# Kernel optimization log

Measured on AMD Instinct MI355X. Metric: run time of the kernel, lower is better.

The kernel has to match this reference:

```python
import jax, jax.numpy as jnp
import numpy as np

HEADS = 16
DIM_HEAD = 64
MASK_VALUE = -(np.finfo(np.float32).max / 2)


def setup_inputs() -> dict:
    key = jax.random.key(0)
    k1, k2, k3 = jax.random.split(key, 3)
    B, N, D = 2, 2048, 1024
    inner = HEADS * DIM_HEAD
    x = jax.random.normal(k1, (B, N, D), dtype=jnp.float32)
    w_qkv = jax.random.normal(k2, (D, 3 * inner), dtype=jnp.float32) * (D ** -0.5)
    w_out = jax.random.normal(k3, (inner, D), dtype=jnp.float32) * (inner ** -0.5)
    b_out = jnp.zeros((D,), dtype=jnp.float32)
    return {"x": x, "w_qkv": w_qkv, "w_out": w_out, "b_out": b_out}


def reference(x, w_qkv, w_out, b_out):
    B, N, D = x.shape
    H, Dh = HEADS, DIM_HEAD
    qkv = x @ w_qkv                                   # [B, N, 3*H*Dh]
    q, k, v = jnp.split(qkv, 3, axis=-1)
    # [B, N, H*Dh] -> [B, H, N, Dh]
    split_heads = lambda t: t.reshape(B, N, H, Dh).transpose(0, 2, 1, 3)
    q, k, v = split_heads(q), split_heads(k), split_heads(v)
    scale = Dh ** -0.5
    sim = jnp.einsum('bhid,bhjd->bhij', q, k) * scale  # [B, H, N, N]
    # causal additive mask: MASK_VALUE above the diagonal
    causal = jnp.triu(jnp.ones((N, N), dtype=bool), k=1)
    mask = jnp.where(causal, jnp.float32(MASK_VALUE), 0.0)
    sim = sim + mask[None, None, :, :]
    attn = jax.nn.softmax(sim, axis=-1)
    out = jnp.einsum('bhij,bhjd->bhid', attn, v)       # [B, H, N, Dh]
    out = out.transpose(0, 2, 1, 3).reshape(B, N, H * Dh)
    return out @ w_out + b_out
```

## Files before the change

### kernel.cpp

```cpp
#include <hip/hip_runtime.h>
#include <hip/hip_bf16.h>

typedef __attribute__((ext_vector_type(4)))  float    f32x4;
typedef __attribute__((ext_vector_type(16))) float    f32x16;
typedef __attribute__((ext_vector_type(8)))  short    bf16x8;
typedef __attribute__((ext_vector_type(4)))  short    s16x4;
typedef __attribute__((ext_vector_type(4)))  unsigned u32x4;

#define B_    2
#define N_    2048
#define D_    1024
#define HEADS 16
#define DH    64
#define M_    4096
#define INNER 1024

static __device__ __forceinline__ short f2bf(float f) {
    __hip_bfloat16 h = __float2bfloat16(f);
    return __builtin_bit_cast(short, h);
}
static __device__ __forceinline__ float bf2f(short s) {
    unsigned u = ((unsigned)(unsigned short)s) << 16;
    return __builtin_bit_cast(float, u);
}
static __device__ __forceinline__ unsigned pack2(float lo, float hi) {
    return ((unsigned)(unsigned short)f2bf(lo)) |
           (((unsigned)(unsigned short)f2bf(hi)) << 16);
}
static __device__ __forceinline__ unsigned cvtpk(float lo, float hi) {
    unsigned r;
    asm("v_cvt_pk_bf16_f32 %0, %1, %2" : "=v"(r) : "v"(lo), "v"(hi));
    return r;
}
static __device__ __forceinline__ void plswap(unsigned& a, unsigned& b) {
    asm("v_permlane32_swap_b32 %0, %1" : "+v"(a), "+v"(b));
}
static __device__ __forceinline__ float fexp2(float x) {
    float r;
    asm("v_exp_f32 %0, %1" : "=v"(r) : "v"(x));
    return r;
}
static __device__ __forceinline__ float flog2(float x) {
    float r;
    asm("v_log_f32 %0, %1" : "=v"(r) : "v"(x));
    return r;
}
static __device__ __forceinline__ float vmax16(f32x16 v) {
    float a = fmaxf(fmaxf(v[0], v[1]), fmaxf(v[2], v[3]));
    float b = fmaxf(fmaxf(v[4], v[5]), fmaxf(v[6], v[7]));
    float c = fmaxf(fmaxf(v[8], v[9]), fmaxf(v[10], v[11]));
    float d = fmaxf(fmaxf(v[12], v[13]), fmaxf(v[14], v[15]));
    return fmaxf(fmaxf(a, b), fmaxf(c, d));
}
static __device__ __forceinline__ float vsum16(f32x16 v) {
    float a = (v[0] + v[1]) + (v[2] + v[3]);
    float b = (v[4] + v[5]) + (v[6] + v[7]);
    float c = (v[8] + v[9]) + (v[10] + v[11]);
    float d = (v[12] + v[13]) + (v[14] + v[15]);
    return (a + b) + (c + d);
}

static __device__ __forceinline__ void transpose_tile(const float* __restrict__ in,
                                                      short* __restrict__ out,
                                                      int R, int C, int bx32, int by32,
                                                      float* t ) {
    int tx = threadIdx.x & 31, ty = threadIdx.x >> 5;
    int bx = bx32 * 32, by = by32 * 32;
#pragma unroll
    for (int j = 0; j < 32; j += 8)
        t[(ty + j) * 33 + tx] = in[(long)(by + ty + j) * C + bx + tx];
    __syncthreads();
#pragma unroll
    for (int j = 0; j < 32; j += 8)
        out[(long)(bx + ty + j) * R + by + tx] = f2bf(t[tx * 33 + ty + j]);
}

__global__ void __launch_bounds__(256) prep_k(const float* __restrict__ x,
                                              short* __restrict__ xb,
                                              const float* __restrict__ w_qkv,
                                              short* __restrict__ wqkvT,
                                              const float* __restrict__ w_out,
                                              short* __restrict__ woutT) {
    __shared__ float t[32 * 33];
    int bid = blockIdx.x;
    if (bid < 4096) {
        int i = bid * 256 + threadIdx.x;
        f32x4 v = ((const f32x4*)x)[i];
        s16x4 o;
        o[0] = f2bf(v[0]); o[1] = f2bf(v[1]); o[2] = f2bf(v[2]); o[3] = f2bf(v[3]);
        ((s16x4*)xb)[i] = o;
    } else if (bid < 4096 + 3072) {
        int tt = bid - 4096;
        transpose_tile(w_qkv, wqkvT, 1024, 3072, tt % 96, tt / 96, t);
    } else {
        int tt = bid - 7168;
        transpose_tile(w_out, woutT, 1024, 1024, tt % 32, tt / 32, t);
    }
}

template <int ROWS>
static __device__ __forceinline__ void stage_swz(const short* __restrict__ src,
                                                 int ldElems, short* lds, int tid) {
    constexpr int CH = (ROWS * 128) / (256 * 16);
#pragma unroll
    for (int c = 0; c < CH; ++c) {
        int o   = (tid + c * 256) * 16;
        int row = o >> 7;
        int kb  = (o & 127) ^ ((row & 7) << 4);
        const char* g = (const char*)src + (long)row * ldElems * 2 + kb;
        __builtin_amdgcn_global_load_lds(
            (const __attribute__((address_space(1))) void*)g,
            (__attribute__((address_space(3))) void*)((char*)lds + o), 16, 0, 0);
    }
}
static __device__ __forceinline__ bf16x8 lds_frag(const short* lds, int row, int kbyte) {
    return *(const bf16x8*)((const char*)lds + (row << 7) + (kbyte ^ ((row & 7) << 4)));
}

__global__ void __launch_bounds__(256) gemm_k(const short* __restrict__ A,
                                              const short* __restrict__ Bt, int K,
                                              short* __restrict__ q_out,
                                              short* __restrict__ k_out,
                                              short* __restrict__ v_out) {
    __shared__ __align__(16) short As[128 * 64];
    __shared__ __align__(16) short Bs[128 * 64];
    int tid = threadIdx.x;
    int lane = tid & 63, w = tid >> 6, wr = w >> 1, wc = w & 1;
    int l15 = lane & 15, lg = lane >> 4;
    int nx = gridDim.x;
    int flat = blockIdx.y * nx + blockIdx.x;
    int total = nx * gridDim.y;
    int cpx = total >> 3;
    int swz = (flat & 7) * cpx + (flat >> 3);
    int row0 = (swz / nx) * 128, col0 = (swz % nx) * 128;

    f32x4 acc[4][4] = {};

    for (int k0 = 0; k0 < K; k0 += 64) {
        stage_swz<128>(A + (long)row0 * K + k0, K, As, tid);
        stage_swz<128>(Bt + (long)col0 * K + k0, K, Bs, tid);
        __syncthreads();
#pragma unroll
        for (int kb = 0; kb < 2; ++kb) {
            int kbyte = kb * 64 + (lg << 4);
            bf16x8 af[4], bfr[4];
#pragma unroll
            for (int mr = 0; mr < 4; ++mr)
                af[mr] = lds_frag(As, wr * 64 + mr * 16 + l15, kbyte);
#pragma unroll
            for (int nr = 0; nr < 4; ++nr)
                bfr[nr] = lds_frag(Bs, wc * 64 + nr * 16 + l15, kbyte);
#pragma unroll
            for (int mr = 0; mr < 4; ++mr)
#pragma unroll
                for (int nr = 0; nr < 4; ++nr)
                    acc[mr][nr] = __builtin_amdgcn_mfma_f32_16x16x32_bf16(
                        af[mr], bfr[nr], acc[mr][nr], 0, 0, 0);
        }
        __syncthreads();
    }

#pragma unroll
    for (int mr = 0; mr < 4; ++mr)
#pragma unroll
        for (int nr = 0; nr < 4; ++nr) {
            int gr0 = row0 + wr * 64 + mr * 16 + (lg << 2);
            int gc  = col0 + wc * 64 + nr * 16 + l15;
            int which = gc >> 10, rem = gc & 1023;
            int h = rem >> 6, d = rem & 63;
            int b = gr0 >> 11, nn0 = gr0 & 2047;
            long bh32 = (long)(b * HEADS + h) * 32;
            if (which == 2) {
                int t = nn0 >> 6, ks = (nn0 >> 4) & 3, hb = (nn0 >> 3) & 1;
                long off = (((bh32 + t) * 2 + (d >> 5)) * 4 + ks) * 512
                           + ((hb << 5) + (d & 31)) * 8 + (nn0 & 4);
                s16x4 pk;
#pragma unroll
                for (int reg = 0; reg < 4; ++reg) pk[reg] = f2bf(acc[mr][nr][reg]);
                *(s16x4*)(v_out + off) = pk;
            } else if (which == 1) {
                int dk = d >> 4, hb = (d >> 3) & 1, j = d & 7;
                int t = nn0 >> 6, ss = (nn0 >> 5) & 1;
                long fbase = ((bh32 + t) * 2 + ss) * 4 + dk;
#pragma unroll
                for (int reg = 0; reg < 4; ++reg) {
                    int l31k = (nn0 + reg) & 31;
                    k_out[fbase * 512 + ((hb << 5) + l31k) * 8 + j] =
                        f2bf(acc[mr][nr][reg]);
                }
            } else {
                float sc = 0.180336880f;
#pragma unroll
                for (int reg = 0; reg < 4; ++reg) {
                    int gr = gr0 + reg;
                    int bb = gr >> 11, nn = gr & 2047;
                    q_out[((long)(bb * HEADS + h) * N_ + nn) * DH + d] =
                        f2bf(acc[mr][nr][reg] * sc);
                }
            }
        }
}

__global__ void __launch_bounds__(256) gemm2_k(const short* __restrict__ A,
                                               const short* __restrict__ Bt,
                                               float* __restrict__ f_out,
                                               const float* __restrict__ bias) {
    __shared__ __align__(16) short As[128 * 64];
    __shared__ __align__(16) short Bs[64 * 64];
    int tid = threadIdx.x;
    int lane = tid & 63, w = tid >> 6, wr = w >> 1, wc = w & 1;
    int l15 = lane & 15, lg = lane >> 4;
    const int K = 1024;
    int flat = blockIdx.y * 16 + blockIdx.x;
    int swz = (flat & 7) * 64 + (flat >> 3);
    int row0 = (swz >> 4) * 128, col0 = (swz & 15) * 64;

    f32x4 acc[4][2] = {};

    for (int k0 = 0; k0 < K; k0 += 64) {
        stage_swz<128>(A + (long)row0 * K + k0, K, As, tid);
        stage_swz<64>(Bt + (long)col0 * K + k0, K, Bs, tid);
        __syncthreads();
#pragma unroll
        for (int kb = 0; kb < 2; ++kb) {
            int kbyte = kb * 64 + (lg << 4);
            bf16x8 af[4], bfr[2];
#pragma unroll
            for (int mr = 0; mr < 4; ++mr)
                af[mr] = lds_frag(As, wr * 64 + mr * 16 + l15, kbyte);
#pragma unroll
            for (int nc = 0; nc < 2; ++nc)
                bfr[nc] = lds_frag(Bs, wc * 32 + nc * 16 + l15, kbyte);
#pragma unroll
            for (int mr = 0; mr < 4; ++mr)
#pragma unroll
                for (int nc = 0; nc < 2; ++nc)
                    acc[mr][nc] = __builtin_amdgcn_mfma_f32_16x16x32_bf16(
                        af[mr], bfr[nc], acc[mr][nc], 0, 0, 0);
        }
        __syncthreads();
    }

#pragma unroll
    for (int mr = 0; mr < 4; ++mr)
#pragma unroll
        for (int nc = 0; nc < 2; ++nc) {
            int gc = col0 + wc * 32 + nc * 16 + l15;
            float bv = bias[gc];
#pragma unroll
            for (int reg = 0; reg < 4; ++reg) {
                int gr = row0 + wr * 64 + mr * 16 + (lg << 2) + reg;
                f_out[(long)gr * D_ + gc] = acc[mr][nc][reg] + bv;
            }
        }
}

__global__ void __launch_bounds__(256, 3) attn_k(const short* __restrict__ Qb,
                                                 const short* __restrict__ Kf,
                                                 const short* __restrict__ Vf,
                                                 short* __restrict__ O0,
                                                 short* __restrict__ O1,
                                                 float* __restrict__ lse) {
    __shared__ __align__(16) short Ep[4][2048];
    int tid = threadIdx.x, lane = tid & 63, w = tid >> 6;
    int l31 = lane & 31, hbit = lane >> 5;
    int bid = blockIdx.x;
    int k8 = bid >> 3;
    int bh = (bid & 7) + ((k8 >> 5) << 3);
    int rest = k8 & 31;
    int q4 = rest >> 3, p = rest & 7;
    int x = (q4 < 2) ? (15 - p) : p;
    int seg = q4 & 1;
    int t0 = seg ? (x + 1) : 0;
    int t1 = seg ? (2 * x + 2) : (x + 1);

    const short* Qh = Qb + (long)bh * N_ * DH;
    const short* Kh = Kf + (long)bh * 32 * 4096;
    const short* Vh = Vf + (long)bh * 32 * 4096;
    int lofs = lane * 8;

    int q0 = x * 128 + w * 32;
    int qg = q0 + l31;
    int t1w = min(t1, ((q0 + 31) >> 6) + 1);

    bf16x8 qf[4];
#pragma unroll
    for (int kf = 0; kf < 4; ++kf)
        qf[kf] = *(const bf16x8*)(Qh + (long)qg * DH + kf * 16 + hbit * 8);

    f32x16 o[2] = {};
    float m = -1e30f, l = 0.f;

    for (int t = t0; t < t1w; ++t) {
        const short* kb = Kh + (long)t * 4096;
        const short* vb = Vh + (long)t * 4096;
        int khb = t * 64;

        bf16x8 kfr[2][4];
#pragma unroll
        for (int ss = 0; ss < 2; ++ss)
#pragma unroll
            for (int dk = 0; dk < 4; ++dk)
                kfr[ss][dk] = *(const bf16x8*)(kb + (ss * 4 + dk) * 512 + lofs);

        f32x16 S[2] = {};
        __builtin_amdgcn_s_setprio(1);
#pragma unroll
        for (int ss = 0; ss < 2; ++ss)
#pragma unroll
            for (int dk = 0; dk < 4; ++dk)
                S[ss] = __builtin_amdgcn_mfma_f32_32x32x16_bf16(
                    kfr[ss][dk], qf[dk], S[ss], 0, 0, 0);
        __builtin_amdgcn_s_setprio(0);

        bf16x8 vf[2][4];
#pragma unroll
        for (int df = 0; df < 2; ++df)
#pragma unroll
            for (int ks = 0; ks < 4; ++ks)
                vf[df][ks] = *(const bf16x8*)(vb + (df * 4 + ks) * 512 + lofs);

        if (khb + 63 > q0) {
            int kvl = khb + 4 * hbit;
#pragma unroll
            for (int ss = 0; ss < 2; ++ss)
#pragma unroll
                for (int r = 0; r < 16; ++r) {
                    int kv = kvl + 32 * ss + (r & 3) + 8 * (r >> 2);
                    if (kv > qg) S[ss][r] = -1e30f;
                }
        }

        float pm = fmaxf(vmax16(S[0]), vmax16(S[1]));
        pm = fmaxf(pm, __shfl_xor(pm, 32));
        if (!__all(pm <= m + 8.0f)) {
            float mn = fmaxf(m, pm);
            float corr = fexp2(m - mn);
            m = mn;
            l *= corr;
#pragma unroll
            for (int df = 0; df < 2; ++df)
#pragma unroll
                for (int r = 0; r < 16; ++r) o[df][r] *= corr;
        }
#pragma unroll
        for (int ss = 0; ss < 2; ++ss)
#pragma unroll
            for (int r = 0; r < 16; ++r)
                S[ss][r] = fexp2(S[ss][r] - m);
        l += vsum16(S[0]) + vsum16(S[1]);

        __builtin_amdgcn_s_setprio(1);
#pragma unroll
        for (int ss = 0; ss < 2; ++ss) {
#pragma unroll
            for (int hs = 0; hs < 2; ++hs) {
                unsigned w0 = cvtpk(S[ss][hs * 8 + 0], S[ss][hs * 8 + 1]);
                unsigned w1 = cvtpk(S[ss][hs * 8 + 2], S[ss][hs * 8 + 3]);
                unsigned w2 = cvtpk(S[ss][hs * 8 + 4], S[ss][hs * 8 + 5]);
                unsigned w3 = cvtpk(S[ss][hs * 8 + 6], S[ss][hs * 8 + 7]);
                plswap(w0, w2);
                plswap(w1, w3);
                bf16x8 pfrag = __builtin_bit_cast(bf16x8, (u32x4){w0, w1, w2, w3});
                int ks = ss * 2 + hs;
#pragma unroll
                for (int df = 0; df < 2; ++df)
                    o[df] = __builtin_amdgcn_mfma_f32_32x32x16_bf16(
                        vf[df][ks], pfrag, o[df], 0, 0, 0);
            }
        }
        __builtin_amdgcn_s_setprio(0);
    }

    l += __shfl_xor(l, 32);
    float linv = (l > 0.f) ? 1.0f / l : 0.f;
    if (hbit == 0)
        lse[seg * (32 * N_) + bh * N_ + qg] =
            (l > 0.f) ? (m + flog2(l)) : -__builtin_inff();

    char* Epw = (char*)&Ep[w][0];
#pragma unroll
    for (int df = 0; df < 2; ++df)
#pragma unroll
        for (int r = 0; r < 16; r += 2) {
            unsigned pk = pack2(o[df][r] * linv, o[df][r + 1] * linv);
            int d = df * 32 + (r & 3) + 8 * (r >> 2) + 4 * hbit;
            int cb = d * 2;
            *(unsigned*)(Epw + (l31 << 7) + (cb ^ ((l31 & 7) << 4))) = pk;
        }
    __syncthreads();

    int b = bh >> 4, h = bh & 15;
    int lr = lane >> 1, lc = lane & 1;
    const char* rbase = Epw + (lr << 7);
    long orow = seg ? ((long)(bh * N_ + q0 + lr)) * 64 + lc * 32
                    : ((long)(b * N_ + q0 + lr)) * INNER + h * DH + lc * 32;
    short* dst = seg ? O1 : O0;
#pragma unroll
    for (int j = 0; j < 4; ++j) {
        int cb = lc * 64 + j * 16;
        bf16x8 vv = *(const bf16x8*)(rbase + (cb ^ ((lr & 7) << 4)));
        *(bf16x8*)(dst + orow + j * 8) = vv;
    }
}

__global__ void __launch_bounds__(256) merge_k(short* __restrict__ Ab,
                                               const short* __restrict__ O1,
                                               const float* __restrict__ lse) {
    int gid = blockIdx.x * 256 + threadIdx.x;
    int row = gid >> 3, d0 = (gid & 7) * 8;
    int bh = row >> 11, n = row & 2047;
    float l0 = lse[row];
    float l1 = lse[32 * N_ + row];
    float Mx = fmaxf(l0, l1);
    float w0 = fexp2(l0 - Mx), w1 = fexp2(l1 - Mx);
    float inv = 1.0f / (w0 + w1);
    w0 *= inv; w1 *= inv;
    int b = bh >> 4, h = bh & 15;
    long a_off = ((long)(b * N_ + n) * HEADS + h) * DH + d0;
    long o_off = (long)row * DH + d0;
    bf16x8 v0 = *(const bf16x8*)(Ab + a_off);
    bf16x8 v1 = *(const bf16x8*)(O1 + o_off);
    bf16x8 r;
#pragma unroll
    for (int i = 0; i < 8; ++i)
        r[i] = f2bf(w0 * bf2f(v0[i]) + w1 * bf2f(v1[i]));
    *(bf16x8*)(Ab + a_off) = r;
}


extern "C" void kernel_launch(void* const* d_in, const int* in_sizes, int n_in,
                              void* d_out, int out_size, void* d_ws, size_t ws_size,
                              hipStream_t stream) {
    const float* x     = (const float*)d_in[0];
    const float* w_qkv = (const float*)d_in[1];
    const float* w_out = (const float*)d_in[2];
    const float* b_out = (const float*)d_in[3];
    float* out = (float*)d_out;

    char* ws = (char*)d_ws;
    const size_t MB = 1024 * 1024;
    short* xb    = (short*)(ws + 0 * MB);
    short* wqkvT = (short*)(ws + 8 * MB);
    short* woutT = (short*)(ws + 14 * MB);
    short* Qb    = (short*)(ws + 16 * MB);
    short* Kfb   = (short*)(ws + 24 * MB);
    short* Vfb   = (short*)(ws + 32 * MB);
    short* Ab    = (short*)(ws + 40 * MB);
    short* O1    = (short*)(ws + 0 * MB);
    float* lse   = (float*)(ws + 8 * MB);

    prep_k<<<dim3(4096 + 3072 + 1024), 256, 0, stream>>>(
        x, xb, w_qkv, wqkvT, w_out, woutT);

    gemm_k<<<dim3(3072 / 128, M_ / 128), 256, 0, stream>>>(
        xb, wqkvT, 1024, Qb, Kfb, Vfb);

    attn_k<<<dim3(1024), 256, 0, stream>>>(Qb, Kfb, Vfb, Ab, O1, lse);
    merge_k<<<dim3((32 * N_ * 8) / 256), 256, 0, stream>>>(Ab, O1, lse);

    gemm2_k<<<dim3(1024 / 64, M_ / 128), 256, 0, stream>>>(Ab, woutT, out, b_out);
}
```

Baseline: 103.7 us.

## Double-buffer K/V tiles in LDS via async global_load_lds in attention

The attention kernel no longer has each wave read K and V fragments straight from global memory. The block now stages each 64-key K/V tile once into shared memory with global_load_lds, double-buffered two tiles ahead, and synchronises with vmcnt waits and barriers. This cuts the fourfold redundant global/L2 traffic across the block's waves and overlaps tile loads with MFMA work. In exchange, shared memory doubles to 32KB, barriers are added per tile, and all waves now run the loop to the block-wide bound, idling on tiles past their own causal limit.

```diff
diff --git a/kernel.cpp b/kernel.cpp
--- a/kernel.cpp
+++ b/kernel.cpp
@@ -255,13 +255,24 @@
         }
 }
 
+static __device__ __forceinline__ void stage16(const short* __restrict__ src,
+                                               short* lds, int tid) {
+#pragma unroll
+    for (int r = 0; r < 2; ++r) {
+        int o = tid * 16 + r * 4096;
+        __builtin_amdgcn_global_load_lds(
+            (const __attribute__((address_space(1))) void*)((const char*)src + o),
+            (__attribute__((address_space(3))) void*)((char*)lds + o), 16, 0, 0);
+    }
+}
+
 __global__ void __launch_bounds__(256, 3) attn_k(const short* __restrict__ Qb,
                                                  const short* __restrict__ Kf,
                                                  const short* __restrict__ Vf,
                                                  short* __restrict__ O0,
                                                  short* __restrict__ O1,
                                                  float* __restrict__ lse) {
-    __shared__ __align__(16) short Ep[4][2048];
+    __shared__ __align__(16) short Sm[16384];
     int tid = threadIdx.x, lane = tid & 63, w = tid >> 6;
     int l31 = lane & 31, hbit = lane >> 5;
     int bid = blockIdx.x;
@@ -291,85 +302,105 @@
     f32x16 o[2] = {};
     float m = -1e30f, l = 0.f;
 
-    for (int t = t0; t < t1w; ++t) {
-        const short* kb = Kh + (long)t * 4096;
-        const short* vb = Vh + (long)t * 4096;
+    stage16(Kh + (long)t0 * 4096, Sm, tid);
+    stage16(Vh + (long)t0 * 4096, Sm + 4096, tid);
+    if (t0 + 1 < t1) {
+        stage16(Kh + (long)(t0 + 1) * 4096, Sm + 8192, tid);
+        stage16(Vh + (long)(t0 + 1) * 4096, Sm + 12288, tid);
+    }
+
+    for (int t = t0; t < t1; ++t) {
+        short* Kls = Sm + ((t - t0) & 1) * 8192;
+        short* Vls = Kls + 4096;
         int khb = t * 64;
 
+        if (t + 1 < t1) asm volatile("s_waitcnt vmcnt(4)" ::: "memory");
+        else            asm volatile("s_waitcnt vmcnt(0)" ::: "memory");
+        __builtin_amdgcn_s_barrier();
+
         bf16x8 kfr[2][4];
 #pragma unroll
         for (int ss = 0; ss < 2; ++ss)
 #pragma unroll
             for (int dk = 0; dk < 4; ++dk)
-                kfr[ss][dk] = *(const bf16x8*)(kb + (ss * 4 + dk) * 512 + lofs);
-
-        f32x16 S[2] = {};
-        __builtin_amdgcn_s_setprio(1);
-#pragma unroll
-        for (int ss = 0; ss < 2; ++ss)
-#pragma unroll
-            for (int dk = 0; dk < 4; ++dk)
-                S[ss] = __builtin_amdgcn_mfma_f32_32x32x16_bf16(
-                    kfr[ss][dk], qf[dk], S[ss], 0, 0, 0);
-        __builtin_amdgcn_s_setprio(0);
-
+                kfr[ss][dk] = *(const bf16x8*)(Kls + (ss * 4 + dk) * 512 + lofs);
         bf16x8 vf[2][4];
 #pragma unroll
         for (int df = 0; df < 2; ++df)
 #pragma unroll
             for (int ks = 0; ks < 4; ++ks)
-                vf[df][ks] = *(const bf16x8*)(vb + (df * 4 + ks) * 512 + lofs);
-
-        if (khb + 63 > q0) {
-            int kvl = khb + 4 * hbit;
+                vf[df][ks] = *(const bf16x8*)(Vls + (df * 4 + ks) * 512 + lofs);
+        asm volatile("s_waitcnt lgkmcnt(0)" ::: "memory");
+        __builtin_amdgcn_sched_barrier(0);
+        __builtin_amdgcn_s_barrier();
+
+        if (t + 2 < t1) {
+            stage16(Kh + (long)(t + 2) * 4096, Kls, tid);
+            stage16(Vh + (long)(t + 2) * 4096, Vls, tid);
+        }
+
+        if (t < t1w) {
+            f32x16 S[2] = {};
+            __builtin_amdgcn_s_setprio(1);
 #pragma unroll
             for (int ss = 0; ss < 2; ++ss)
 #pragma unroll
-                for (int r = 0; r < 16; ++r) {
-                    int kv = kvl + 32 * ss + (r & 3) + 8 * (r >> 2);
-                    if (kv > qg) S[ss][r] = -1e30f;
+                for (int dk = 0; dk < 4; ++dk)
+                    S[ss] = __builtin_amdgcn_mfma_f32_32x32x16_bf16(
+                        kfr[ss][dk], qf[dk], S[ss], 0, 0, 0);
+            __builtin_amdgcn_s_setprio(0);
+
+            if (khb + 63 > q0) {
+                int kvl = khb + 4 * hbit;
+#pragma unroll
+                for (int ss = 0; ss < 2; ++ss)
+#pragma unroll
+                    for (int r = 0; r < 16; ++r) {
+                        int kv = kvl + 32 * ss + (r & 3) + 8 * (r >> 2);
+                        if (kv > qg) S[ss][r] = -1e30f;
+                    }
+            }
+
+            float pm = fmaxf(vmax16(S[0]), vmax16(S[1]));
+            pm = fmaxf(pm, __shfl_xor(pm, 32));
+            if (!__all(pm <= m + 8.0f)) {
+                float mn = fmaxf(m, pm);
+                float corr = fexp2(m - mn);
+                m = mn;
+                l *= corr;
+#pragma unroll
+                for (int df = 0; df < 2; ++df)
+#pragma unroll
+                    for (int r = 0; r < 16; ++r) o[df][r] *= corr;
+            }
+#pragma unroll
+            for (int ss = 0; ss < 2; ++ss)
+#pragma unroll
+                for (int r = 0; r < 16; ++r)
+                    S[ss][r] = fexp2(S[ss][r] - m);
+            l += vsum16(S[0]) + vsum16(S[1]);
+
+            __builtin_amdgcn_s_setprio(1);
+#pragma unroll
+            for (int ss = 0; ss < 2; ++ss) {
+#pragma unroll
+                for (int hs = 0; hs < 2; ++hs) {
+                    unsigned w0 = cvtpk(S[ss][hs * 8 + 0], S[ss][hs * 8 + 1]);
+                    unsigned w1 = cvtpk(S[ss][hs * 8 + 2], S[ss][hs * 8 + 3]);
+                    unsigned w2 = cvtpk(S[ss][hs * 8 + 4], S[ss][hs * 8 + 5]);
+                    unsigned w3 = cvtpk(S[ss][hs * 8 + 6], S[ss][hs * 8 + 7]);
+                    plswap(w0, w2);
+                    plswap(w1, w3);
+                    bf16x8 pfrag = __builtin_bit_cast(bf16x8, (u32x4){w0, w1, w2, w3});
+                    int ks = ss * 2 + hs;
+#pragma unroll
+                    for (int df = 0; df < 2; ++df)
+                        o[df] = __builtin_amdgcn_mfma_f32_32x32x16_bf16(
+                            vf[df][ks], pfrag, o[df], 0, 0, 0);
                 }
-        }
-
-        float pm = fmaxf(vmax16(S[0]), vmax16(S[1]));
-        pm = fmaxf(pm, __shfl_xor(pm, 32));
-        if (!__all(pm <= m + 8.0f)) {
-            float mn = fmaxf(m, pm);
-            float corr = fexp2(m - mn);
-            m = mn;
-            l *= corr;
-#pragma unroll
-            for (int df = 0; df < 2; ++df)
-#pragma unroll
-                for (int r = 0; r < 16; ++r) o[df][r] *= corr;
-        }
-#pragma unroll
-        for (int ss = 0; ss < 2; ++ss)
-#pragma unroll
-            for (int r = 0; r < 16; ++r)
-                S[ss][r] = fexp2(S[ss][r] - m);
-        l += vsum16(S[0]) + vsum16(S[1]);
-
-        __builtin_amdgcn_s_setprio(1);
-#pragma unroll
-        for (int ss = 0; ss < 2; ++ss) {
-#pragma unroll
-            for (int hs = 0; hs < 2; ++hs) {
-                unsigned w0 = cvtpk(S[ss][hs * 8 + 0], S[ss][hs * 8 + 1]);
-                unsigned w1 = cvtpk(S[ss][hs * 8 + 2], S[ss][hs * 8 + 3]);
-                unsigned w2 = cvtpk(S[ss][hs * 8 + 4], S[ss][hs * 8 + 5]);
-                unsigned w3 = cvtpk(S[ss][hs * 8 + 6], S[ss][hs * 8 + 7]);
-                plswap(w0, w2);
-                plswap(w1, w3);
-                bf16x8 pfrag = __builtin_bit_cast(bf16x8, (u32x4){w0, w1, w2, w3});
-                int ks = ss * 2 + hs;
-#pragma unroll
-                for (int df = 0; df < 2; ++df)
-                    o[df] = __builtin_amdgcn_mfma_f32_32x32x16_bf16(
-                        vf[df][ks], pfrag, o[df], 0, 0, 0);
             }
-        }
-        __builtin_amdgcn_s_setprio(0);
+            __builtin_amdgcn_s_setprio(0);
+        }
     }
 
     l += __shfl_xor(l, 32);
@@ -378,7 +409,7 @@
         lse[seg * (32 * N_) + bh * N_ + qg] =
             (l > 0.f) ? (m + flog2(l)) : -__builtin_inff();
 
-    char* Epw = (char*)&Ep[w][0];
+    char* Epw = (char*)(Sm + w * 2048);
 #pragma unroll
     for (int df = 0; df < 2; ++df)
 #pragma unroll
```

New measurement: 103.5 us. No clear change (-0.1%).
